# Kernel tuning notes

Hardware: AMD Instinct MI355X
Metric: run time of the kernel (lower is better)

Reference implementation:

```python
import jax, jax.numpy as jnp
import numpy as np
from jax import lax

IMG = 512
STRIDES = (4, 8, 16, 32)
SIZES = (32.0, 64.0, 128.0, 256.0)
PRE_NMS = 1000
POST_NMS = 300
NMS_THR = 0.7
NCLS = 12


def conv(x, w, b, stride=1):
    y = lax.conv_general_dilated(x, w, (stride, stride), 'SAME',
                                 dimension_numbers=('NCHW', 'OIHW', 'NCHW'))
    return y + b[None, :, None, None]


def relu(x):
    return jax.nn.relu(x)


def up2(x):
    return jnp.repeat(jnp.repeat(x, 2, axis=2), 2, axis=3)


def make_anchors(hf, wf, stride, size):
    ratios = jnp.array([0.5, 1.0, 2.0], jnp.float32)
    hr = jnp.sqrt(ratios)
    ws = size / hr
    hs = size * hr
    cx = (jnp.arange(wf, dtype=jnp.float32) + 0.5) * stride
    cy = (jnp.arange(hf, dtype=jnp.float32) + 0.5) * stride
    cyg, cxg = jnp.meshgrid(cy, cx, indexing='ij')
    x1 = cxg[..., None] - ws / 2; y1 = cyg[..., None] - hs / 2
    x2 = cxg[..., None] + ws / 2; y2 = cyg[..., None] + hs / 2
    return jnp.stack([x1, y1, x2, y2], -1).reshape(-1, 4)  # [hf*wf*3, 4]


def decode(anchors, deltas):
    aw = anchors[..., 2] - anchors[..., 0]
    ah = anchors[..., 3] - anchors[..., 1]
    acx = anchors[..., 0] + aw * 0.5
    acy = anchors[..., 1] + ah * 0.5
    dx, dy, dw, dh = (deltas[..., 0], deltas[..., 1], deltas[..., 2], deltas[..., 3])
    lim = 4.135  # log(1000/16), as in torchvision
    dw = jnp.clip(dw, -lim, lim); dh = jnp.clip(dh, -lim, lim)
    cx = dx * aw + acx; cy = dy * ah + acy
    w = aw * jnp.exp(dw); h = ah * jnp.exp(dh)
    boxes = jnp.stack([cx - w / 2, cy - h / 2, cx + w / 2, cy + h / 2], -1)
    return jnp.clip(boxes, 0.0, float(IMG))


def iou_one(box, boxes):
    x1 = jnp.maximum(box[0], boxes[:, 0]); y1 = jnp.maximum(box[1], boxes[:, 1])
    x2 = jnp.minimum(box[2], boxes[:, 2]); y2 = jnp.minimum(box[3], boxes[:, 3])
    inter = jnp.maximum(x2 - x1, 0.0) * jnp.maximum(y2 - y1, 0.0)
    a = (box[2] - box[0]) * (box[3] - box[1])
    b = (boxes[:, 2] - boxes[:, 0]) * (boxes[:, 3] - boxes[:, 1])
    return inter / jnp.maximum(a + b - inter, 1e-6)


def nms(boxes, scores, thr, k):
    def body(i, state):
        s, keep = state
        idx = jnp.argmax(s)
        keep = keep.at[i].set(idx.astype(jnp.int32))
        ious = iou_one(boxes[idx], boxes)
        s = jnp.where(ious > thr, -jnp.inf, s)  # also removes the picked box
        return s, keep
    keep = jnp.zeros((k,), jnp.int32)
    _, keep = lax.fori_loop(0, k, body, (scores, keep))
    return keep


def roi_align(feat, rois, scale, out=7, sr=2):
    # feat: [C,H,W]; rois: [R,4] in image coords; sampling_ratio=2, avg pooling
    C, H, W = feat.shape
    R = rois.shape[0]
    b = rois * scale
    x1, y1 = b[:, 0], b[:, 1]
    bw = jnp.maximum(b[:, 2] - x1, 1.0) / out
    bh = jnp.maximum(b[:, 3] - y1, 1.0) / out
    off = (jnp.arange(sr, dtype=jnp.float32) + 0.5) / sr
    grid = jnp.arange(out, dtype=jnp.float32)[:, None] + off[None, :]  # [out,sr]
    ys = (y1[:, None, None] + grid[None] * bh[:, None, None]).reshape(R, out * sr)
    xs = (x1[:, None, None] + grid[None] * bw[:, None, None]).reshape(R, out * sr)
    ys = jnp.clip(ys, 0.0, H - 1.0)
    xs = jnp.clip(xs, 0.0, W - 1.0)
    y0 = jnp.floor(ys).astype(jnp.int32); y1i = jnp.minimum(y0 + 1, H - 1)
    x0 = jnp.floor(xs).astype(jnp.int32); x1i = jnp.minimum(x0 + 1, W - 1)
    wy1 = ys - y0.astype(jnp.float32); wy0 = 1.0 - wy1
    wx1 = xs - x0.astype(jnp.float32); wx0 = 1.0 - wx1
    def g(yi, xi):
        return feat[:, yi[:, :, None], xi[:, None, :]]  # [C,R,S,S]
    val = (wy0[:, :, None] * wx0[:, None, :])[None] * g(y0, x0) \
        + (wy0[:, :, None] * wx1[:, None, :])[None] * g(y0, x1i) \
        + (wy1[:, :, None] * wx0[:, None, :])[None] * g(y1i, x0) \
        + (wy1[:, :, None] * wx1[:, None, :])[None] * g(y1i, x1i)
    val = val.reshape(C, R, out, sr, out, sr).mean(axis=(3, 5))
    return val.transpose(1, 0, 2, 3)  # [R,C,out,out]


def _forward(images, stem_w, stem_b, c2_w, c2_b, c3_w, c3_b, c4_w, c4_b, c5_w, c5_b,
             lat2_w, lat2_b, lat3_w, lat3_b, lat4_w, lat4_b, lat5_w, lat5_b,
             fpn2_w, fpn2_b, fpn3_w, fpn3_b, fpn4_w, fpn4_b, fpn5_w, fpn5_b,
             rpn_w, rpn_b, rpncls_w, rpncls_b, rpnreg_w, rpnreg_b,
             fc1_w, fc1_b, fc2_w, fc2_b, cls_w, cls_b, reg_w, reg_b):
    B = images.shape[0]
    # --- backbone (ResNet50-FPN channel plan, collapsed residual stages) ---
    x = relu(conv(images, stem_w, stem_b, 2))                      # [B,64,256,256]
    x = lax.reduce_window(x, -jnp.inf, lax.max, (1, 1, 3, 3), (1, 1, 2, 2), 'SAME')
    c2 = relu(conv(x, c2_w, c2_b, 1))                              # [B,256,128,128]
    c3 = relu(conv(c2, c3_w, c3_b, 2))                             # [B,512,64,64]
    c4 = relu(conv(c3, c4_w, c4_b, 2))                             # [B,1024,32,32]
    c5 = relu(conv(c4, c5_w, c5_b, 2))                             # [B,2048,16,16]
    # --- FPN ---
    p5 = conv(c5, lat5_w, lat5_b)
    p4 = conv(c4, lat4_w, lat4_b) + up2(p5)
    p3 = conv(c3, lat3_w, lat3_b) + up2(p4)
    p2 = conv(c2, lat2_w, lat2_b) + up2(p3)
    p2 = conv(p2, fpn2_w, fpn2_b); p3 = conv(p3, fpn3_w, fpn3_b)
    p4 = conv(p4, fpn4_w, fpn4_b); p5 = conv(p5, fpn5_w, fpn5_b)
    feats = [p2, p3, p4, p5]
    # --- RPN: objectness/deltas per level, decode, per-level top-k ---
    all_s, all_b = [], []
    for feat, stride, size in zip(feats, STRIDES, SIZES):
        hf, wf = feat.shape[2], feat.shape[3]
        anchors = make_anchors(hf, wf, stride, size)
        t = relu(conv(feat, rpn_w, rpn_b))
        logits = conv(t, rpncls_w, rpncls_b).transpose(0, 2, 3, 1).reshape(B, -1)
        deltas = conv(t, rpnreg_w, rpnreg_b).transpose(0, 2, 3, 1).reshape(B, -1, 4)
        boxes = decode(anchors[None], deltas)
        k = min(PRE_NMS, logits.shape[1])
        s, idx = lax.top_k(logits, k)
        bsel = jnp.take_along_axis(boxes, jnp.broadcast_to(idx[:, :, None], (B, k, 4)), axis=1)
        all_s.append(s); all_b.append(bsel)
    scores = jnp.concatenate(all_s, axis=1)
    boxes = jnp.concatenate(all_b, axis=1)
    # --- NMS -> fixed 300 proposals per image ---
    def per_image(bx, sc):
        keep = nms(bx, sc, NMS_THR, POST_NMS)
        return bx[keep]
    proposals = jax.vmap(per_image)(boxes, scores)  # [B,300,4]
    # --- multi-level ROIAlign (FPN level assignment) ---
    def per_image_pool(f2, f3, f4, f5, props):
        area = jnp.maximum((props[:, 2] - props[:, 0]) * (props[:, 3] - props[:, 1]), 1e-6)
        lvl = jnp.clip(jnp.floor(4.0 + jnp.log2(jnp.sqrt(area) / 224.0)), 2.0, 5.0).astype(jnp.int32) - 2
        pooled = jnp.zeros((props.shape[0], f2.shape[0], 7, 7), f2.dtype)
        for l, (f, sc) in enumerate(zip((f2, f3, f4, f5), (0.25, 0.125, 0.0625, 0.03125))):
            pooled = pooled + jnp.where((lvl == l)[:, None, None, None], roi_align(f, props, sc), 0.0)
        return pooled
    pooled = jax.vmap(per_image_pool)(p2, p3, p4, p5, proposals)  # [B,300,256,7,7]
    # --- box head ---
    h = pooled.reshape(B * POST_NMS, -1)
    h = relu(h @ fc1_w.T + fc1_b)
    h = relu(h @ fc2_w.T + fc2_b)
    cls = h @ cls_w.T + cls_b            # [B*300, 12]
    reg = h @ reg_w.T + reg_b            # [B*300, 48]
    return jnp.concatenate([cls, reg], axis=-1)  # [B*300, 60]


def setup_inputs() -> dict:
    key = jax.random.key(0)
    ks = iter(jax.random.split(key, 64))
    def w(shape, scale=0.05):
        return jax.random.normal(next(ks), shape, jnp.float32) * scale
    d = {}
    d['images'] = jax.random.normal(next(ks), (1, 3, IMG, IMG), jnp.float32)
    d['stem_w'] = w((64, 3, 7, 7)); d['stem_b'] = jnp.zeros((64,), jnp.float32)
    d['c2_w'] = w((256, 64, 3, 3)); d['c2_b'] = jnp.zeros((256,), jnp.float32)
    d['c3_w'] = w((512, 256, 3, 3)); d['c3_b'] = jnp.zeros((512,), jnp.float32)
    d['c4_w'] = w((1024, 512, 3, 3)); d['c4_b'] = jnp.zeros((1024,), jnp.float32)
    d['c5_w'] = w((2048, 1024, 3, 3)); d['c5_b'] = jnp.zeros((2048,), jnp.float32)
    for name, cin in (('lat2', 256), ('lat3', 512), ('lat4', 1024), ('lat5', 2048)):
        d[name + '_w'] = w((256, cin, 1, 1)); d[name + '_b'] = jnp.zeros((256,), jnp.float32)
    for name in ('fpn2', 'fpn3', 'fpn4', 'fpn5'):
        d[name + '_w'] = w((256, 256, 3, 3)); d[name + '_b'] = jnp.zeros((256,), jnp.float32)
    d['rpn_w'] = w((256, 256, 3, 3)); d['rpn_b'] = jnp.zeros((256,), jnp.float32)
    d['rpncls_w'] = w((3, 256, 1, 1)); d['rpncls_b'] = jnp.zeros((3,), jnp.float32)
    d['rpnreg_w'] = w((12, 256, 1, 1)); d['rpnreg_b'] = jnp.zeros((12,), jnp.float32)
    d['fc1_w'] = w((1024, 256 * 49), 0.01); d['fc1_b'] = jnp.zeros((1024,), jnp.float32)
    d['fc2_w'] = w((1024, 1024), 0.02); d['fc2_b'] = jnp.zeros((1024,), jnp.float32)
    d['cls_w'] = w((NCLS, 1024), 0.02); d['cls_b'] = jnp.zeros((NCLS,), jnp.float32)
    d['reg_w'] = w((4 * NCLS, 1024), 0.02); d['reg_b'] = jnp.zeros((4 * NCLS,), jnp.float32)
    return d


def reference(images, stem_w, stem_b, c2_w, c2_b, c3_w, c3_b, c4_w, c4_b, c5_w, c5_b,
              lat2_w, lat2_b, lat3_w, lat3_b, lat4_w, lat4_b, lat5_w, lat5_b,
              fpn2_w, fpn2_b, fpn3_w, fpn3_b, fpn4_w, fpn4_b, fpn5_w, fpn5_b,
              rpn_w, rpn_b, rpncls_w, rpncls_b, rpnreg_w, rpnreg_b,
              fc1_w, fc1_b, fc2_w, fc2_b, cls_w, cls_b, reg_w, reg_b):
    return _forward(images, stem_w, stem_b, c2_w, c2_b, c3_w, c3_b, c4_w, c4_b, c5_w, c5_b,
                    lat2_w, lat2_b, lat3_w, lat3_b, lat4_w, lat4_b, lat5_w, lat5_b,
                    fpn2_w, fpn2_b, fpn3_w, fpn3_b, fpn4_w, fpn4_b, fpn5_w, fpn5_b,
                    rpn_w, rpn_b, rpncls_w, rpncls_b, rpnreg_w, rpnreg_b,
                    fc1_w, fc1_b, fc2_w, fc2_b, cls_w, cls_b, reg_w, reg_b)
```

## Files before the change

kernel.cpp:

```cpp
#include <hip/hip_runtime.h>
#include <math.h>


#define NSEL 3768
#define MWORDS 60

__device__ __forceinline__ unsigned key32(float f) {
  unsigned u = __float_as_uint(f);
  return (u & 0x80000000u) ? ~u : (u | 0x80000000u);
}

template<int K, int STRIDE, int TW, int TH, int BK, int PADLO, int MCO>
__global__ __launch_bounds__(256) void conv_tile(
    const float* __restrict__ in, const float* __restrict__ wgt,
    const float* __restrict__ bias, float* __restrict__ out,
    int Cin, int Hin, int Win, int Hout, int Wout, int do_relu,
    const float* __restrict__ up)
{
  constexpr int CO  = 16 * MCO;
  constexpr int PC  = TW * STRIDE + (K - STRIDE);
  constexpr int PR  = TH * STRIDE + (K - STRIDE);
  constexpr int PCP = (PC + 3) & ~3;
  constexpr int KK  = K * K;
  constexpr int SEG = 4 * STRIDE + (K - STRIDE);
  constexpr int PTOT = BK * PR * PCP;

  __shared__ __align__(16) float patch[BK][PR][PCP];
  __shared__ __align__(16) float wlds[BK][KK][CO];

  const int tid = threadIdx.x;
  const int tx = tid & 15, ty = tid >> 4;
  const int tilesW = Wout / TW;
  const int tw = blockIdx.x % tilesW, th = blockIdx.x / tilesW;
  const int OW0 = tw * TW, OH0 = th * TH;
  const int co_base = blockIdx.y * CO;
  const int sp0 = tx * 4;
  const int ow0 = sp0 % TW, oh0 = sp0 / TW;
  const int IW0 = OW0 * STRIDE - PADLO;
  const int IH0 = OH0 * STRIDE - PADLO;

  float acc[MCO][4];
#pragma unroll
  for (int i = 0; i < MCO; ++i) {
    float bv = bias[co_base + ty * MCO + i];
#pragma unroll
    for (int j = 0; j < 4; ++j) acc[i][j] = bv;
  }

  const int nk = Cin / BK;
  for (int ks = 0; ks < nk; ++ks) {
    const int cib = ks * BK;
    for (int e = tid; e < PTOT; e += 256) {
      int ci = e / (PR * PCP);
      int r  = (e / PCP) % PR;
      int pc = e % PCP;
      int gy = IH0 + r, gx = IW0 + pc;
      float v = 0.0f;
      if (pc < PC && (unsigned)gy < (unsigned)Hin && (unsigned)gx < (unsigned)Win)
        v = in[((size_t)(cib + ci) * Hin + gy) * Win + gx];
      ((float*)patch)[e] = v;
    }
    for (int p = tid; p < BK * CO; p += 256) {
      int co = p % CO, ci = p / CO;
      const float* wp = wgt + ((size_t)(co_base + co) * Cin + (cib + ci)) * KK;
#pragma unroll
      for (int k = 0; k < KK; ++k) wlds[ci][k][co] = wp[k];
    }
    __syncthreads();

#pragma unroll
    for (int ci = 0; ci < BK; ++ci) {
#pragma unroll
      for (int kh = 0; kh < K; ++kh) {
        float bseg[SEG];
        const float* bp = &patch[ci][oh0 * STRIDE + kh][ow0 * STRIDE];
        if constexpr (SEG == 4) {
          float4 t = *reinterpret_cast<const float4*>(bp);
          bseg[0] = t.x; bseg[1] = t.y; bseg[2] = t.z; bseg[3] = t.w;
        } else if constexpr (SEG == 6) {
          float4 t = *reinterpret_cast<const float4*>(bp);
          float2 u = *reinterpret_cast<const float2*>(bp + 4);
          bseg[0] = t.x; bseg[1] = t.y; bseg[2] = t.z; bseg[3] = t.w;
          bseg[4] = u.x; bseg[5] = u.y;
        } else if constexpr (SEG == 9) {
          float4 t = *reinterpret_cast<const float4*>(bp);
          float4 u = *reinterpret_cast<const float4*>(bp + 4);
          bseg[0] = t.x; bseg[1] = t.y; bseg[2] = t.z; bseg[3] = t.w;
          bseg[4] = u.x; bseg[5] = u.y; bseg[6] = u.z; bseg[7] = u.w;
          bseg[8] = bp[8];
        } else if constexpr (SEG == 13) {
          float4 t = *reinterpret_cast<const float4*>(bp);
          float4 u = *reinterpret_cast<const float4*>(bp + 4);
          float4 v = *reinterpret_cast<const float4*>(bp + 8);
          bseg[0] = t.x; bseg[1] = t.y; bseg[2] = t.z; bseg[3] = t.w;
          bseg[4] = u.x; bseg[5] = u.y; bseg[6] = u.z; bseg[7] = u.w;
          bseg[8] = v.x; bseg[9] = v.y; bseg[10] = v.z; bseg[11] = v.w;
          bseg[12] = bp[12];
        }
#pragma unroll
        for (int kw = 0; kw < K; ++kw) {
          float a[MCO];
          if constexpr (MCO == 4) {
            float4 av = *reinterpret_cast<const float4*>(&wlds[ci][kh * K + kw][ty * 4]);
            a[0] = av.x; a[1] = av.y; a[2] = av.z; a[3] = av.w;
          } else {
            a[0] = wlds[ci][kh * K + kw][ty];
          }
#pragma unroll
          for (int j = 0; j < 4; ++j) {
            float b = bseg[j * STRIDE + kw];
#pragma unroll
            for (int i = 0; i < MCO; ++i)
              acc[i][j] = fmaf(a[i], b, acc[i][j]);
          }
        }
      }
    }
    __syncthreads();
  }

  const int oh = OH0 + oh0;
#pragma unroll
  for (int i = 0; i < MCO; ++i) {
    int co = co_base + ty * MCO + i;
#pragma unroll
    for (int j = 0; j < 4; ++j) {
      int ow = OW0 + ow0 + j;
      float v = acc[i][j];
      if (up) {
        int H2 = Hout >> 1, W2 = Wout >> 1;
        v += up[((size_t)co * H2 + (oh >> 1)) * W2 + (ow >> 1)];
      }
      if (do_relu) v = fmaxf(v, 0.0f);
      out[((size_t)co * Hout + oh) * Wout + ow] = v;
    }
  }
}

__global__ __launch_bounds__(256) void maxpool_kernel(
    const float* __restrict__ in, float* __restrict__ out)
{
  int c = blockIdx.z;
  int w = blockIdx.x * 16 + threadIdx.x;
  int h = blockIdx.y * 16 + threadIdx.y;
  if (w >= 128 || h >= 128) return;
  const float* p = in + (size_t)c * 256 * 256;
  float m = -INFINITY;
  for (int kh = 0; kh < 3; ++kh) {
    int hi = h * 2 + kh;
    if (hi < 256)
      for (int kw = 0; kw < 3; ++kw) {
        int wi = w * 2 + kw;
        if (wi < 256) m = fmaxf(m, p[hi * 256 + wi]);
      }
  }
  out[((size_t)c * 128 + h) * 128 + w] = m;
}

__global__ __launch_bounds__(256) void rpn_head_kernel(
    const float* __restrict__ t,
    const float* __restrict__ clsw, const float* __restrict__ clsb,
    const float* __restrict__ regw, const float* __restrict__ regb,
    float* __restrict__ scores, float* __restrict__ boxes,
    int H, int W, int stride, float asize, int base)
{
  int idx = blockIdx.x * blockDim.x + threadIdx.x;
  int n = H * W * 3;
  if (idx >= n) return;
  int a = idx % 3;
  int pos = idx / 3;
  int wp = pos % W, hp = pos / W;
  size_t hw = (size_t)H * W;
  const float* tp = t + (size_t)hp * W + wp;
  const float* cw = clsw + a * 256;
  const float* rw0 = regw + (a * 4 + 0) * 256;
  const float* rw1 = regw + (a * 4 + 1) * 256;
  const float* rw2 = regw + (a * 4 + 2) * 256;
  const float* rw3 = regw + (a * 4 + 3) * 256;
  float s = clsb[a];
  float d0 = regb[a * 4 + 0], d1 = regb[a * 4 + 1];
  float d2 = regb[a * 4 + 2], d3 = regb[a * 4 + 3];
  for (int c = 0; c < 256; ++c) {
    float v = tp[c * hw];
    s = fmaf(v, cw[c], s);
    d0 = fmaf(v, rw0[c], d0);
    d1 = fmaf(v, rw1[c], d1);
    d2 = fmaf(v, rw2[c], d2);
    d3 = fmaf(v, rw3[c], d3);
  }
  float r = (a == 0) ? 0.5f : ((a == 1) ? 1.0f : 2.0f);
  float hr = sqrtf(r);
  float ws = asize / hr, hs = asize * hr;
  float cx0 = ((float)wp + 0.5f) * (float)stride;
  float cy0 = ((float)hp + 0.5f) * (float)stride;
  float ax1 = cx0 - ws * 0.5f, ax2 = cx0 + ws * 0.5f;
  float ay1 = cy0 - hs * 0.5f, ay2 = cy0 + hs * 0.5f;
  float aw = ax2 - ax1, ah = ay2 - ay1;
  float acx = ax1 + aw * 0.5f, acy = ay1 + ah * 0.5f;
  float dw = fminf(fmaxf(d2, -4.135f), 4.135f);
  float dh = fminf(fmaxf(d3, -4.135f), 4.135f);
  float cx = d0 * aw + acx;
  float cy = d1 * ah + acy;
  float bw = aw * expf(dw);
  float bh = ah * expf(dh);
  float x1 = fminf(fmaxf(cx - bw * 0.5f, 0.0f), 512.0f);
  float y1 = fminf(fmaxf(cy - bh * 0.5f, 0.0f), 512.0f);
  float x2 = fminf(fmaxf(cx + bw * 0.5f, 0.0f), 512.0f);
  float y2 = fminf(fmaxf(cy + bh * 0.5f, 0.0f), 512.0f);
  scores[base + idx] = s;
  float* bp = boxes + 4 * (size_t)(base + idx);
  bp[0] = x1; bp[1] = y1; bp[2] = x2; bp[3] = y2;
}

__global__ __launch_bounds__(256) void topk_kernel(
    const float* __restrict__ scores_all, const float* __restrict__ boxes_all,
    float* __restrict__ sel_s, float* __restrict__ sel_b)
{
  const int offs[5] = {0, 49152, 61440, 64512, 65280};
  const int kks[4]  = {1000, 1000, 1000, 768};
  const int soff[4] = {0, 1000, 2000, 3000};
  int l = blockIdx.x;
  int lo = offs[l], n = offs[l + 1] - lo, k = kks[l], so = soff[l];
  int tid = threadIdx.x;

  if (k >= n) {
    for (int i = tid; i < n; i += blockDim.x) {
      sel_s[so + i] = scores_all[lo + i];
      const float* bp = boxes_all + 4 * (size_t)(lo + i);
      float* op = sel_b + 4 * (size_t)(so + i);
      op[0] = bp[0]; op[1] = bp[1]; op[2] = bp[2]; op[3] = bp[3];
    }
    return;
  }

  __shared__ unsigned hist[256];
  __shared__ unsigned sh_prefix, sh_mask;
  __shared__ int sh_k, cnt1, cnt2;
  if (tid == 0) { sh_prefix = 0u; sh_mask = 0u; sh_k = k; cnt1 = 0; cnt2 = 0; }
  __syncthreads();

  for (int p = 3; p >= 0; --p) {
    hist[tid] = 0u;
    __syncthreads();
    unsigned pre = sh_prefix, msk = sh_mask;
    for (int i = tid; i < n; i += blockDim.x) {
      unsigned u = key32(scores_all[lo + i]);
      if ((u & msk) == pre)
        atomicAdd(&hist[(u >> (p * 8)) & 255u], 1u);
    }
    __syncthreads();
    if (tid == 0) {
      int rem = sh_k, b;
      for (b = 255; b >= 0; --b) {
        int c = (int)hist[b];
        if (rem <= c) break;
        rem -= c;
      }
      if (b < 0) b = 0;
      sh_k = rem;
      sh_prefix |= ((unsigned)b << (p * 8));
      sh_mask |= (255u << (p * 8));
    }
    __syncthreads();
  }
  unsigned T = sh_prefix;

  for (int i = tid; i < n; i += blockDim.x) {
    float sc = scores_all[lo + i];
    if (key32(sc) > T) {
      int pos = atomicAdd(&cnt1, 1);
      sel_s[so + pos] = sc;
      const float* bp = boxes_all + 4 * (size_t)(lo + i);
      float* op = sel_b + 4 * (size_t)(so + pos);
      op[0] = bp[0]; op[1] = bp[1]; op[2] = bp[2]; op[3] = bp[3];
    }
  }
  __syncthreads();
  int ngreater = cnt1;
  for (int i = tid; i < n; i += blockDim.x) {
    float sc = scores_all[lo + i];
    if (key32(sc) == T) {
      int pos = atomicAdd(&cnt2, 1);
      if (ngreater + pos < k) {
        sel_s[so + ngreater + pos] = sc;
        const float* bp = boxes_all + 4 * (size_t)(lo + i);
        float* op = sel_b + 4 * (size_t)(so + ngreater + pos);
        op[0] = bp[0]; op[1] = bp[1]; op[2] = bp[2]; op[3] = bp[3];
      }
    }
  }
}

__global__ __launch_bounds__(256) void nms_mask_kernel(
    const float* __restrict__ sel_b, unsigned long long* __restrict__ mask)
{
  int wid = (blockIdx.x * 256 + threadIdx.x) >> 6;
  int lane = threadIdx.x & 63;
  if (wid >= NSEL) return;
  const float* bb = sel_b + 4 * (size_t)wid;
  float bx1 = bb[0], by1 = bb[1], bx2 = bb[2], by2 = bb[3];
  float barea = (bx2 - bx1) * (by2 - by1);
  unsigned long long* row = mask + (size_t)wid * MWORDS;
  for (int w = 0; w < MWORDS; ++w) {
    int j = w * 64 + lane;
    bool sup = false;
    if (j < NSEL) {
      const float* pB = sel_b + 4 * (size_t)j;
      float px1 = pB[0], py1 = pB[1], px2 = pB[2], py2 = pB[3];
      float ix1 = fmaxf(bx1, px1), iy1 = fmaxf(by1, py1);
      float ix2 = fminf(bx2, px2), iy2 = fminf(by2, py2);
      float inter = fmaxf(ix2 - ix1, 0.0f) * fmaxf(iy2 - iy1, 0.0f);
      float areab = (px2 - px1) * (py2 - py1);
      float iou = inter / fmaxf(barea + areab - inter, 1e-6f);
      sup = iou > 0.7f;
    }
    unsigned long long bal = __ballot(sup);
    if (lane == 0) row[w] = bal;
  }
}

__global__ __launch_bounds__(512) void nms_seq_kernel(
    const float* __restrict__ sel_s, const float* __restrict__ sel_b,
    const unsigned long long* __restrict__ mask, float* __restrict__ props)
{
  __shared__ float s[NSEL];
  __shared__ float wv[8];
  __shared__ int wi[8];
  __shared__ int cur;
  int tid = threadIdx.x;
  for (int i = tid; i < NSEL; i += 512) s[i] = sel_s[i];
  __syncthreads();

  for (int it = 0; it < 300; ++it) {
    float bv = -INFINITY;
    int bi = 0x7fffffff;
#pragma unroll
    for (int k = 0; k < 8; ++k) {
      int e = tid + k * 512;
      if (e < NSEL) {
        float v = s[e];
        if (v > bv || (v == bv && e < bi)) { bv = v; bi = e; }
      }
    }
    for (int off = 32; off >= 1; off >>= 1) {
      float ov = __shfl_down(bv, off);
      int oi = __shfl_down(bi, off);
      if (ov > bv || (ov == bv && oi < bi)) { bv = ov; bi = oi; }
    }
    int wave = tid >> 6;
    if ((tid & 63) == 0) { wv[wave] = bv; wi[wave] = bi; }
    __syncthreads();
    if (tid == 0) {
      float v0 = wv[0]; int i0 = wi[0];
      for (int q = 1; q < 8; ++q)
        if (wv[q] > v0 || (wv[q] == v0 && wi[q] < i0)) { v0 = wv[q]; i0 = wi[q]; }
      cur = i0;
    }
    __syncthreads();
    int c = cur;
    if (tid < 4) props[it * 4 + tid] = sel_b[4 * (size_t)c + tid];
    const unsigned long long* row = mask + (size_t)c * MWORDS;
#pragma unroll
    for (int k = 0; k < 8; ++k) {
      int e = tid + k * 512;
      if (e < NSEL) {
        if ((row[e >> 6] >> (e & 63)) & 1ull) s[e] = -INFINITY;
      }
    }
    __syncthreads();
  }
}

__global__ __launch_bounds__(256) void roi_align_kernel(
    const float* __restrict__ props,
    const float* __restrict__ f2, const float* __restrict__ f3,
    const float* __restrict__ f4, const float* __restrict__ f5,
    float* __restrict__ fcin)
{
  int r = blockIdx.x;
  const float* bp = props + 4 * (size_t)r;
  float x1 = bp[0], y1 = bp[1], x2 = bp[2], y2 = bp[3];
  float area = fmaxf((x2 - x1) * (y2 - y1), 1e-6f);
  float lf = floorf(4.0f + log2f(sqrtf(area) / 224.0f));
  lf = fminf(fmaxf(lf, 2.0f), 5.0f);
  int lvl = (int)lf - 2;
  const float* feat; int H; float scale;
  if (lvl == 0)      { feat = f2; H = 128; scale = 0.25f; }
  else if (lvl == 1) { feat = f3; H = 64;  scale = 0.125f; }
  else if (lvl == 2) { feat = f4; H = 32;  scale = 0.0625f; }
  else               { feat = f5; H = 16;  scale = 0.03125f; }
  int W = H;

  __shared__ int   sy0[14], sy1[14], sx0[14], sx1[14];
  __shared__ float swy0[14], swy1[14], swx0[14], swx1[14];
  int tid = threadIdx.x;
  if (tid < 28) {
    int j = tid % 14;
    bool isx = tid >= 14;
    float b1 = (isx ? x1 : y1) * scale;
    float b2 = (isx ? x2 : y2) * scale;
    float bs = fmaxf(b2 - b1, 1.0f) * (1.0f / 7.0f);
    float g = (float)(j >> 1) + ((j & 1) ? 0.75f : 0.25f);
    float coord = b1 + g * bs;
    coord = fminf(fmaxf(coord, 0.0f), (float)(H - 1));
    int c0 = (int)floorf(coord);
    int c1 = min(c0 + 1, H - 1);
    float w1 = coord - (float)c0;
    if (isx) { sx0[j] = c0; sx1[j] = c1; swx1[j] = w1; swx0[j] = 1.0f - w1; }
    else     { sy0[j] = c0; sy1[j] = c1; swy1[j] = w1; swy0[j] = 1.0f - w1; }
  }
  __syncthreads();

  int c = tid;
  const float* fp = feat + (size_t)c * H * W;
  float* op = fcin + (size_t)r * 12544 + (size_t)c * 49;
  for (int oh = 0; oh < 7; ++oh) {
    for (int ow = 0; ow < 7; ++ow) {
      float acc = 0.0f;
#pragma unroll
      for (int sy = 0; sy < 2; ++sy) {
        int i = oh * 2 + sy;
        int yy0 = sy0[i], yy1 = sy1[i];
        float wy0 = swy0[i], wy1 = swy1[i];
#pragma unroll
        for (int sx = 0; sx < 2; ++sx) {
          int j = ow * 2 + sx;
          int xx0 = sx0[j], xx1 = sx1[j];
          float wx0 = swx0[j], wx1 = swx1[j];
          float v = wy0 * wx0 * fp[yy0 * W + xx0]
                  + wy0 * wx1 * fp[yy0 * W + xx1]
                  + wy1 * wx0 * fp[yy1 * W + xx0]
                  + wy1 * wx1 * fp[yy1 * W + xx1];
          acc += v;
        }
      }
      op[oh * 7 + ow] = acc * 0.25f;
    }
  }
}

__global__ __launch_bounds__(256) void gemm_splitk(
    const float* __restrict__ A, const float* __restrict__ B,
    float* __restrict__ part, int M, int N, int K, int klen)
{
  __shared__ float As[16][66];
  __shared__ float Bs[16][66];
  int tid = threadIdx.x;
  int tx = tid % 16, ty = tid / 16;
  int m0 = blockIdx.y * 64, n0 = blockIdx.x * 64;
  int kc = blockIdx.z;
  int kt0 = kc * klen, kt1 = kt0 + klen;
  float acc[4][4] = {};
  for (int kt = kt0; kt < kt1; kt += 16) {
#pragma unroll
    for (int i = 0; i < 4; ++i) {
      int flat = tid + 256 * i;
      int mm = flat >> 4, kk = flat & 15;
      int m = m0 + mm;
      As[kk][mm] = (m < M) ? A[(size_t)m * K + kt + kk] : 0.0f;
      int nn = n0 + mm;
      Bs[kk][mm] = (nn < N) ? B[(size_t)nn * K + kt + kk] : 0.0f;
    }
    __syncthreads();
#pragma unroll
    for (int kk = 0; kk < 16; ++kk) {
      float av[4], bv[4];
#pragma unroll
      for (int i = 0; i < 4; ++i) av[i] = As[kk][ty * 4 + i];
#pragma unroll
      for (int j = 0; j < 4; ++j) bv[j] = Bs[kk][tx * 4 + j];
#pragma unroll
      for (int i = 0; i < 4; ++i)
#pragma unroll
        for (int j = 0; j < 4; ++j)
          acc[i][j] = fmaf(av[i], bv[j], acc[i][j]);
    }
    __syncthreads();
  }
  float* pslab = part + (size_t)kc * M * N;
#pragma unroll
  for (int i = 0; i < 4; ++i) {
    int m = m0 + ty * 4 + i;
    if (m >= M) continue;
#pragma unroll
    for (int j = 0; j < 4; ++j) {
      int n = n0 + tx * 4 + j;
      if (n >= N) continue;
      pslab[(size_t)m * N + n] = acc[i][j];
    }
  }
}

__global__ __launch_bounds__(256) void reduce_bias_relu(
    const float* __restrict__ part, int nchunk,
    const float* __restrict__ bias, float* __restrict__ C,
    int MN, int N, int do_relu)
{
  int idx = blockIdx.x * 256 + threadIdx.x;
  if (idx >= MN) return;
  float v = bias[idx % N];
  for (int c = 0; c < nchunk; ++c) v += part[(size_t)c * MN + idx];
  if (do_relu) v = fmaxf(v, 0.0f);
  C[idx] = v;
}

__global__ __launch_bounds__(256) void heads_kernel(
    const float* __restrict__ h,
    const float* __restrict__ clsw, const float* __restrict__ clsb,
    const float* __restrict__ regw, const float* __restrict__ regb,
    float* __restrict__ out)
{
  int idx = blockIdx.x * blockDim.x + threadIdx.x;
  if (idx >= 300 * 60) return;
  int r = idx / 60, o = idx % 60;
  const float* wrow = (o < 12) ? (clsw + (size_t)o * 1024)
                               : (regw + (size_t)(o - 12) * 1024);
  float acc = (o < 12) ? clsb[o] : regb[o - 12];
  const float* hr = h + (size_t)r * 1024;
  for (int k = 0; k < 1024; ++k) acc = fmaf(hr[k], wrow[k], acc);
  out[idx] = acc;
}

extern "C" void kernel_launch(void* const* d_in, const int* in_sizes, int n_in,
                              void* d_out, int out_size, void* d_ws, size_t ws_size,
                              hipStream_t stream) {
  const float* images  = (const float*)d_in[0];
  const float* stem_w  = (const float*)d_in[1];
  const float* stem_b  = (const float*)d_in[2];
  const float* c2_w    = (const float*)d_in[3];
  const float* c2_b    = (const float*)d_in[4];
  const float* c3_w    = (const float*)d_in[5];
  const float* c3_b    = (const float*)d_in[6];
  const float* c4_w    = (const float*)d_in[7];
  const float* c4_b    = (const float*)d_in[8];
  const float* c5_w    = (const float*)d_in[9];
  const float* c5_b    = (const float*)d_in[10];
  const float* lat2_w  = (const float*)d_in[11];
  const float* lat2_b  = (const float*)d_in[12];
  const float* lat3_w  = (const float*)d_in[13];
  const float* lat3_b  = (const float*)d_in[14];
  const float* lat4_w  = (const float*)d_in[15];
  const float* lat4_b  = (const float*)d_in[16];
  const float* lat5_w  = (const float*)d_in[17];
  const float* lat5_b  = (const float*)d_in[18];
  const float* fpn2_w  = (const float*)d_in[19];
  const float* fpn2_b  = (const float*)d_in[20];
  const float* fpn3_w  = (const float*)d_in[21];
  const float* fpn3_b  = (const float*)d_in[22];
  const float* fpn4_w  = (const float*)d_in[23];
  const float* fpn4_b  = (const float*)d_in[24];
  const float* fpn5_w  = (const float*)d_in[25];
  const float* fpn5_b  = (const float*)d_in[26];
  const float* rpn_w   = (const float*)d_in[27];
  const float* rpn_b   = (const float*)d_in[28];
  const float* rpncls_w = (const float*)d_in[29];
  const float* rpncls_b = (const float*)d_in[30];
  const float* rpnreg_w = (const float*)d_in[31];
  const float* rpnreg_b = (const float*)d_in[32];
  const float* fc1_w   = (const float*)d_in[33];
  const float* fc1_b   = (const float*)d_in[34];
  const float* fc2_w   = (const float*)d_in[35];
  const float* fc2_b   = (const float*)d_in[36];
  const float* cls_w   = (const float*)d_in[37];
  const float* cls_b   = (const float*)d_in[38];
  const float* reg_w   = (const float*)d_in[39];
  const float* reg_b   = (const float*)d_in[40];

  const size_t NEED = 18677760ull * 4ull;
  if (ws_size < NEED) return;
  float* ws = (float*)d_ws;
  float* STEM = ws;
  float* POOL = ws + 4194304;
  float* C2   = ws + 5242880;
  float* C3   = ws + 9437184;
  float* C4   = ws + 11534336;
  float* C5   = ws + 12582912;
  float* LAT2 = ws + 13107200;
  float* LAT3 = ws + 17301504;
  float* LAT4 = ws + 18350080;
  float* LAT5 = ws + 18612224;
  float* SCORES = POOL;
  float* BOXES  = POOL + 65280;
  float* SELS   = POOL + 326400;
  float* SELB   = POOL + 330168;
  float* PROPS  = POOL + 345240;
  float* FC1O   = POOL + 346440;
  float* FC2O   = POOL + 653640;
  float* FCIN = STEM;
  float* RPNT = LAT2;
  float* PART1 = C2;
  float* PART2 = C3;
  unsigned long long* MASKS = (unsigned long long*)RPNT;

  dim3 b16(16, 16);

  conv_tile<7,2,16,4,3,2,4><<<dim3(1024, 1), 256, 0, stream>>>(
      images, stem_w, stem_b, STEM, 3, 512, 512, 256, 256, 1, nullptr);
  maxpool_kernel<<<dim3(8, 8, 64), b16, 0, stream>>>(STEM, POOL);
  conv_tile<3,1,64,1,8,1,4><<<dim3(256, 4), 256, 0, stream>>>(
      POOL, c2_w, c2_b, C2, 64, 128, 128, 128, 128, 1, nullptr);
  conv_tile<3,2,64,1,8,0,4><<<dim3(64, 8), 256, 0, stream>>>(
      C2, c3_w, c3_b, C3, 256, 128, 128, 64, 64, 1, nullptr);
  conv_tile<3,2,32,2,8,0,1><<<dim3(16, 64), 256, 0, stream>>>(
      C3, c4_w, c4_b, C4, 512, 64, 64, 32, 32, 1, nullptr);
  conv_tile<3,2,16,4,8,0,1><<<dim3(4, 128), 256, 0, stream>>>(
      C4, c5_w, c5_b, C5, 1024, 32, 32, 16, 16, 1, nullptr);

  conv_tile<1,1,16,4,8,0,4><<<dim3(4, 4), 256, 0, stream>>>(
      C5, lat5_w, lat5_b, LAT5, 2048, 16, 16, 16, 16, 0, nullptr);
  conv_tile<1,1,32,2,8,0,4><<<dim3(16, 4), 256, 0, stream>>>(
      C4, lat4_w, lat4_b, LAT4, 1024, 32, 32, 32, 32, 0, LAT5);
  conv_tile<1,1,64,1,8,0,4><<<dim3(64, 4), 256, 0, stream>>>(
      C3, lat3_w, lat3_b, LAT3, 512, 64, 64, 64, 64, 0, LAT4);
  conv_tile<1,1,64,1,8,0,4><<<dim3(256, 4), 256, 0, stream>>>(
      C2, lat2_w, lat2_b, LAT2, 256, 128, 128, 128, 128, 0, LAT3);

  conv_tile<3,1,64,1,8,1,4><<<dim3(256, 4), 256, 0, stream>>>(
      LAT2, fpn2_w, fpn2_b, C2, 256, 128, 128, 128, 128, 0, nullptr);
  conv_tile<3,1,64,1,8,1,4><<<dim3(64, 4), 256, 0, stream>>>(
      LAT3, fpn3_w, fpn3_b, C3, 256, 64, 64, 64, 64, 0, nullptr);
  conv_tile<3,1,32,2,8,1,4><<<dim3(16, 4), 256, 0, stream>>>(
      LAT4, fpn4_w, fpn4_b, C4, 256, 32, 32, 32, 32, 0, nullptr);
  conv_tile<3,1,16,4,8,1,4><<<dim3(4, 4), 256, 0, stream>>>(
      LAT5, fpn5_w, fpn5_b, C5, 256, 16, 16, 16, 16, 0, nullptr);

  conv_tile<3,1,64,1,8,1,4><<<dim3(256, 4), 256, 0, stream>>>(
      C2, rpn_w, rpn_b, RPNT, 256, 128, 128, 128, 128, 1, nullptr);
  rpn_head_kernel<<<(49152 + 255) / 256, 256, 0, stream>>>(
      RPNT, rpncls_w, rpncls_b, rpnreg_w, rpnreg_b, SCORES, BOXES,
      128, 128, 4, 32.0f, 0);
  conv_tile<3,1,64,1,8,1,4><<<dim3(64, 4), 256, 0, stream>>>(
      C3, rpn_w, rpn_b, RPNT, 256, 64, 64, 64, 64, 1, nullptr);
  rpn_head_kernel<<<(12288 + 255) / 256, 256, 0, stream>>>(
      RPNT, rpncls_w, rpncls_b, rpnreg_w, rpnreg_b, SCORES, BOXES,
      64, 64, 8, 64.0f, 49152);
  conv_tile<3,1,32,2,8,1,4><<<dim3(16, 4), 256, 0, stream>>>(
      C4, rpn_w, rpn_b, RPNT, 256, 32, 32, 32, 32, 1, nullptr);
  rpn_head_kernel<<<(3072 + 255) / 256, 256, 0, stream>>>(
      RPNT, rpncls_w, rpncls_b, rpnreg_w, rpnreg_b, SCORES, BOXES,
      32, 32, 16, 128.0f, 61440);
  conv_tile<3,1,16,4,8,1,4><<<dim3(4, 4), 256, 0, stream>>>(
      C5, rpn_w, rpn_b, RPNT, 256, 16, 16, 16, 16, 1, nullptr);
  rpn_head_kernel<<<(768 + 255) / 256, 256, 0, stream>>>(
      RPNT, rpncls_w, rpncls_b, rpnreg_w, rpnreg_b, SCORES, BOXES,
      16, 16, 32, 256.0f, 64512);

  topk_kernel<<<4, 256, 0, stream>>>(SCORES, BOXES, SELS, SELB);
  nms_mask_kernel<<<(NSEL * 64 + 255) / 256, 256, 0, stream>>>(SELB, MASKS);
  nms_seq_kernel<<<1, 512, 0, stream>>>(SELS, SELB, MASKS, PROPS);

  roi_align_kernel<<<300, 256, 0, stream>>>(PROPS, C2, C3, C4, C5, FCIN);

  gemm_splitk<<<dim3(16, 5, 8), 256, 0, stream>>>(
      FCIN, fc1_w, PART1, 300, 1024, 12544, 1568);
  reduce_bias_relu<<<(307200 + 255) / 256, 256, 0, stream>>>(
      PART1, 8, fc1_b, FC1O, 307200, 1024, 1);
  gemm_splitk<<<dim3(16, 5, 4), 256, 0, stream>>>(
      FC1O, fc2_w, PART2, 300, 1024, 1024, 256);
  reduce_bias_relu<<<(307200 + 255) / 256, 256, 0, stream>>>(
      PART2, 4, fc2_b, FC2O, 307200, 1024, 1);
  heads_kernel<<<(18000 + 255) / 256, 256, 0, stream>>>(
      FC2O, cls_w, cls_b, reg_w, reg_b, (float*)d_out);
}
```

Measured before the change: 5.836 ms.

## Add one-output-per-thread strided conv kernel for deep backbone stages

Adds a conv_deep kernel for the 3x3 stride-2 convolutions c3, c4 and c5. Each wavefront computes one output channel over a 16x4 spatial tile, with one output pixel per thread. Input patches and weights are staged in shared memory in chunks of 8 channels. This greatly raises the number of blocks for the deep low-resolution layers to improve occupancy and parallelism. The cost is much less register reuse: every thread reloads the whole patch per output channel, so shared-memory traffic per FMA goes up.

After: 6.640 ms. 1.14x slower.

```diff
diff --git a/kernel.cpp b/kernel.cpp
--- a/kernel.cpp
+++ b/kernel.cpp
@@ -135,6 +135,72 @@
       out[((size_t)co * Hout + oh) * Wout + ow] = v;
     }
   }
+}
+
+template<int BK>
+__global__ __launch_bounds__(256) void conv_deep(
+    const float* __restrict__ in, const float* __restrict__ wgt,
+    const float* __restrict__ bias, float* __restrict__ out,
+    int Cin, int Hin, int Win, int Hout, int Wout)
+{
+  constexpr int TW = 16, TH = 4;
+  constexpr int PR = TH * 2 + 1;
+  constexpr int PC = TW * 2 + 1;
+  constexpr int PCP = (PC + 3) & ~3;
+  constexpr int PTOT = BK * PR * PCP;
+
+  __shared__ __align__(16) float patch[BK][PR][PCP];
+  __shared__ float wlds[4][BK][9];
+
+  const int tid = threadIdx.x;
+  const int lane = tid & 63, w = tid >> 6;
+  const int ow = lane & 15, oh = lane >> 4;
+  const int tilesW = Wout / TW;
+  const int tw = blockIdx.x % tilesW, th = blockIdx.x / tilesW;
+  const int OW0 = tw * TW, OH0 = th * TH;
+  const int co = blockIdx.y * 4 + w;
+  const int IW0 = OW0 * 2, IH0 = OH0 * 2;
+
+  float acc = bias[co];
+
+  const int nk = Cin / BK;
+  for (int ks = 0; ks < nk; ++ks) {
+    const int cib = ks * BK;
+    for (int e = tid; e < PTOT; e += 256) {
+      int ci = e / (PR * PCP);
+      int r  = (e / PCP) % PR;
+      int pc = e % PCP;
+      int gy = IH0 + r, gx = IW0 + pc;
+      float v = 0.0f;
+      if (pc < PC && gy < Hin && gx < Win)
+        v = in[((size_t)(cib + ci) * Hin + gy) * Win + gx];
+      ((float*)patch)[e] = v;
+    }
+    for (int p = tid; p < 4 * BK * 9; p += 256) {
+      int ww = p / (BK * 9), rem = p % (BK * 9);
+      int ci = rem / 9, k = rem % 9;
+      wlds[ww][ci][k] =
+          wgt[((size_t)(blockIdx.y * 4 + ww) * Cin + cib + ci) * 9 + k];
+    }
+    __syncthreads();
+
+#pragma unroll
+    for (int ci = 0; ci < BK; ++ci) {
+#pragma unroll
+      for (int kh = 0; kh < 3; ++kh) {
+        const float* row = &patch[ci][oh * 2 + kh][ow * 2];
+        float2 v01 = *reinterpret_cast<const float2*>(row);
+        float v2 = row[2];
+        acc = fmaf(v01.x, wlds[w][ci][kh * 3 + 0], acc);
+        acc = fmaf(v01.y, wlds[w][ci][kh * 3 + 1], acc);
+        acc = fmaf(v2,    wlds[w][ci][kh * 3 + 2], acc);
+      }
+    }
+    __syncthreads();
+  }
+
+  acc = fmaxf(acc, 0.0f);
+  out[((size_t)co * Hout + OH0 + oh) * Wout + OW0 + ow] = acc;
 }
 
 __global__ __launch_bounds__(256) void maxpool_kernel(
@@ -599,12 +665,12 @@
   maxpool_kernel<<<dim3(8, 8, 64), b16, 0, stream>>>(STEM, POOL);
   conv_tile<3,1,64,1,8,1,4><<<dim3(256, 4), 256, 0, stream>>>(
       POOL, c2_w, c2_b, C2, 64, 128, 128, 128, 128, 1, nullptr);
-  conv_tile<3,2,64,1,8,0,4><<<dim3(64, 8), 256, 0, stream>>>(
-      C2, c3_w, c3_b, C3, 256, 128, 128, 64, 64, 1, nullptr);
-  conv_tile<3,2,32,2,8,0,1><<<dim3(16, 64), 256, 0, stream>>>(
-      C3, c4_w, c4_b, C4, 512, 64, 64, 32, 32, 1, nullptr);
-  conv_tile<3,2,16,4,8,0,1><<<dim3(4, 128), 256, 0, stream>>>(
-      C4, c5_w, c5_b, C5, 1024, 32, 32, 16, 16, 1, nullptr);
+  conv_deep<8><<<dim3(64, 128), 256, 0, stream>>>(
+      C2, c3_w, c3_b, C3, 256, 128, 128, 64, 64);
+  conv_deep<8><<<dim3(16, 256), 256, 0, stream>>>(
+      C3, c4_w, c4_b, C4, 512, 64, 64, 32, 32);
+  conv_deep<8><<<dim3(4, 512), 256, 0, stream>>>(
+      C4, c5_w, c5_b, C5, 1024, 32, 32, 16, 16);
 
   conv_tile<1,1,16,4,8,0,4><<<dim3(4, 4), 256, 0, stream>>>(
       C5, lat5_w, lat5_b, LAT5, 2048, 16, 16, 16, 16, 0, nullptr);
```

## Replace strided 3x3 backbone convs with split-K implicit GEMM plus reduction

Applied to the files above, without the earlier changes.

The stride-2 3x3 convolutions for c3, c4 and c5 move from the direct tiled conv kernel to an implicit-GEMM kernel. It uses 64x64 shared-memory tiles with an im2col gather, and the K dimension is split across blockIdx.z so the deep, spatially small layers launch more blocks. A separate reduce kernel sums the partial slabs, adds the bias and applies ReLU. This is meant to raise occupancy and data reuse on the deep layers, at the cost of extra global traffic for the partials, extra launches, and per-element integer divides in the gather.

Result: faster. 4.900 ms (-16.0%).

```diff
diff --git a/kernel.cpp b/kernel.cpp
--- a/kernel.cpp
+++ b/kernel.cpp
@@ -135,6 +135,81 @@
       out[((size_t)co * Hout + oh) * Wout + ow] = v;
     }
   }
+}
+
+template<int WSHIFT>
+__global__ __launch_bounds__(256) void conv_igemm(
+    const float* __restrict__ in, const float* __restrict__ wgt,
+    float* __restrict__ part, int Hin, int Win, int Nsp, int K, int kchunk)
+{
+  __shared__ float As[16][66];
+  __shared__ float Bs[16][66];
+  int tid = threadIdx.x;
+  int tx = tid % 16, ty = tid / 16;
+  int m0 = blockIdx.y * 64, n0 = blockIdx.x * 64;
+  int kc = blockIdx.z;
+  int kt0 = kc * kchunk, kt1 = kt0 + kchunk;
+  float acc[4][4] = {};
+  for (int kt = kt0; kt < kt1; kt += 16) {
+#pragma unroll
+    for (int i = 0; i < 4; ++i) {
+      int flat = tid + 256 * i;
+      int mm = flat >> 4, kk = flat & 15;
+      As[kk][mm] = wgt[(size_t)(m0 + mm) * K + kt + kk];
+    }
+#pragma unroll
+    for (int i = 0; i < 4; ++i) {
+      int flat = tid + 256 * i;
+      int nn = flat & 63, kk = flat >> 6;
+      int kabs = kt + kk;
+      int ci = kabs / 9, r = kabs % 9;
+      int kh = r / 3, kw = r % 3;
+      int nabs = n0 + nn;
+      int oh = nabs >> WSHIFT, ow = nabs & ((1 << WSHIFT) - 1);
+      int iy = oh * 2 + kh, ix = ow * 2 + kw;
+      float v = 0.0f;
+      if (iy < Hin && ix < Win)
+        v = in[((size_t)ci * Hin + iy) * Win + ix];
+      Bs[kk][nn] = v;
+    }
+    __syncthreads();
+#pragma unroll
+    for (int kk = 0; kk < 16; ++kk) {
+      float av[4], bv[4];
+#pragma unroll
+      for (int i = 0; i < 4; ++i) av[i] = As[kk][ty * 4 + i];
+#pragma unroll
+      for (int j = 0; j < 4; ++j) bv[j] = Bs[kk][tx * 4 + j];
+#pragma unroll
+      for (int i = 0; i < 4; ++i)
+#pragma unroll
+        for (int j = 0; j < 4; ++j)
+          acc[i][j] = fmaf(av[i], bv[j], acc[i][j]);
+    }
+    __syncthreads();
+  }
+  float* pslab = part + (size_t)blockIdx.z * gridDim.y * 64 * Nsp;
+#pragma unroll
+  for (int i = 0; i < 4; ++i) {
+    int m = m0 + ty * 4 + i;
+#pragma unroll
+    for (int j = 0; j < 4; ++j) {
+      int n = n0 + tx * 4 + j;
+      pslab[(size_t)m * Nsp + n] = acc[i][j];
+    }
+  }
+}
+
+__global__ __launch_bounds__(256) void reduce_conv(
+    const float* __restrict__ part, int nchunk,
+    const float* __restrict__ bias, float* __restrict__ C,
+    int MN, int NSHIFT)
+{
+  int idx = blockIdx.x * 256 + threadIdx.x;
+  if (idx >= MN) return;
+  float v = bias[idx >> NSHIFT];
+  for (int c = 0; c < nchunk; ++c) v += part[(size_t)c * MN + idx];
+  C[idx] = fmaxf(v, 0.0f);
 }
 
 __global__ __launch_bounds__(256) void maxpool_kernel(
@@ -588,6 +663,7 @@
   float* FC2O   = POOL + 653640;
   float* FCIN = STEM;
   float* RPNT = LAT2;
+  float* CPART = LAT2;
   float* PART1 = C2;
   float* PART2 = C3;
   unsigned long long* MASKS = (unsigned long long*)RPNT;
@@ -599,12 +675,19 @@
   maxpool_kernel<<<dim3(8, 8, 64), b16, 0, stream>>>(STEM, POOL);
   conv_tile<3,1,64,1,8,1,4><<<dim3(256, 4), 256, 0, stream>>>(
       POOL, c2_w, c2_b, C2, 64, 128, 128, 128, 128, 1, nullptr);
-  conv_tile<3,2,64,1,8,0,4><<<dim3(64, 8), 256, 0, stream>>>(
-      C2, c3_w, c3_b, C3, 256, 128, 128, 64, 64, 1, nullptr);
-  conv_tile<3,2,32,2,8,0,1><<<dim3(16, 64), 256, 0, stream>>>(
-      C3, c4_w, c4_b, C4, 512, 64, 64, 32, 32, 1, nullptr);
-  conv_tile<3,2,16,4,8,0,1><<<dim3(4, 128), 256, 0, stream>>>(
-      C4, c5_w, c5_b, C5, 1024, 32, 32, 16, 16, 1, nullptr);
+
+  conv_igemm<6><<<dim3(64, 8, 2), 256, 0, stream>>>(
+      C2, c3_w, CPART, 128, 128, 4096, 2304, 1152);
+  reduce_conv<<<(2097152 + 255) / 256, 256, 0, stream>>>(
+      CPART, 2, c3_b, C3, 2097152, 12);
+  conv_igemm<5><<<dim3(16, 16, 4), 256, 0, stream>>>(
+      C3, c4_w, CPART, 64, 64, 1024, 4608, 1152);
+  reduce_conv<<<(1048576 + 255) / 256, 256, 0, stream>>>(
+      CPART, 4, c4_b, C4, 1048576, 10);
+  conv_igemm<4><<<dim3(4, 32, 8), 256, 0, stream>>>(
+      C4, c5_w, CPART, 32, 32, 256, 9216, 1152);
+  reduce_conv<<<(524288 + 255) / 256, 256, 0, stream>>>(
+      CPART, 8, c5_b, C5, 524288, 8);
 
   conv_tile<1,1,16,4,8,0,4><<<dim3(4, 4), 256, 0, stream>>>(
       C5, lat5_w, lat5_b, LAT5, 2048, 16, 16, 16, 16, 0, nullptr);
```
